# Performance work log

Measured on AMD Instinct MI355X. Metric: run time of the kernel, lower is better.

## Reference

```python
import jax, jax.numpy as jnp
import numpy as np

B, Q, K, QSIZE, KSIZE, H, VDIM = 4, 1024, 1024, 256, 256, 32, 256


def setup_inputs() -> dict:
    key = jax.random.key(0)
    ks = jax.random.split(key, 10)
    return {
        "keys": jax.random.normal(ks[0], (B, K, KSIZE), dtype=jnp.float32),
        "queries": jax.random.normal(ks[1], (B, Q, QSIZE), dtype=jnp.float32),
        "values": jax.random.normal(ks[2], (B, K, VDIM), dtype=jnp.float32),
        "valid_lens": jax.random.randint(ks[3], (B,), 1, K + 1, dtype=jnp.int32),
        "W_q": jax.random.normal(ks[4], (QSIZE, H), dtype=jnp.float32) * (QSIZE ** -0.5),
        "b_q": jnp.zeros((H,), dtype=jnp.float32),
        "W_k": jax.random.normal(ks[5], (KSIZE, H), dtype=jnp.float32) * (KSIZE ** -0.5),
        "b_k": jnp.zeros((H,), dtype=jnp.float32),
        "w_v": jax.random.normal(ks[6], (H,), dtype=jnp.float32) * (H ** -0.5),
        "b_v": jnp.zeros((), dtype=jnp.float32),
    }


def reference(keys, queries, values, valid_lens, W_q, b_q, W_k, b_k, w_v, b_v):
    # projected features: (B,K,H) and (B,Q,H)
    fk = keys @ W_k + b_k
    fq = queries @ W_q + b_q
    # broadcast add -> (B,Q,K,H), tanh, then scalar projection -> scores (B,Q,K)
    features = jnp.tanh(fq[:, :, None, :] + fk[:, None, :, :])
    scores = jnp.einsum("bqkh,h->bqk", features, w_v) + b_v
    # masked softmax over key axis: positions >= valid_len get -1e6
    mask = jnp.arange(K)[None, None, :] < valid_lens[:, None, None]
    scores = jnp.where(mask, scores, jnp.float32(-1e6))
    weights = jax.nn.softmax(scores, axis=-1)
    # bmm: (B,Q,K) @ (B,K,V) -> (B,Q,V)
    return jnp.einsum("bqk,bkv->bqv", weights, values)
```

## Files before the change

kernel.cpp:

```cpp
#include <hip/hip_runtime.h>
#include <math.h>


#define NB 4
#define NQ 1024
#define NK 1024
#define DQK 256
#define NH 32
#define NV 256
#define TQ 8
#define BLK 512

__device__ __forceinline__ float fast_rcp(float x) { return __builtin_amdgcn_rcpf(x); }

__global__ __launch_bounds__(256) void proj_kernel(
    const float* __restrict__ queries, const float* __restrict__ keys,
    const float* __restrict__ W_q, const float* __restrict__ b_q,
    const float* __restrict__ W_k, const float* __restrict__ b_k,
    float* __restrict__ eq, float* __restrict__ ek)
{
    const int tid     = blockIdx.x * 256 + threadIdx.x;
    const int row     = tid >> 5;
    const int sub     = tid & 31;
    const int h4      = (sub & 7) * 4;
    const int quarter = sub >> 3;

    const float* src; const float* W; const float* bias; float* dst; int r;
    if (row < NB * NQ) { r = row;           src = queries + (size_t)r * DQK; W = W_q; bias = b_q; dst = eq; }
    else               { r = row - NB * NQ; src = keys    + (size_t)r * DQK; W = W_k; bias = b_k; dst = ek; }

    float a0 = 0.f, a1 = 0.f, a2 = 0.f, a3 = 0.f;
    if (quarter == 0) {
        float4 bv4 = *(const float4*)(bias + h4);
        a0 = bv4.x; a1 = bv4.y; a2 = bv4.z; a3 = bv4.w;
    }
    const int d0 = quarter * 64;
    #pragma unroll 4
    for (int i = d0; i < d0 + 64; i += 4) {
        float4 s  = *(const float4*)(src + i);
        float4 w0 = *(const float4*)(W + (size_t)(i + 0) * NH + h4);
        float4 w1 = *(const float4*)(W + (size_t)(i + 1) * NH + h4);
        float4 w2 = *(const float4*)(W + (size_t)(i + 2) * NH + h4);
        float4 w3 = *(const float4*)(W + (size_t)(i + 3) * NH + h4);
        a0 = fmaf(s.x, w0.x, a0); a1 = fmaf(s.x, w0.y, a1); a2 = fmaf(s.x, w0.z, a2); a3 = fmaf(s.x, w0.w, a3);
        a0 = fmaf(s.y, w1.x, a0); a1 = fmaf(s.y, w1.y, a1); a2 = fmaf(s.y, w1.z, a2); a3 = fmaf(s.y, w1.w, a3);
        a0 = fmaf(s.z, w2.x, a0); a1 = fmaf(s.z, w2.y, a1); a2 = fmaf(s.z, w2.z, a2); a3 = fmaf(s.z, w2.w, a3);
        a0 = fmaf(s.w, w3.x, a0); a1 = fmaf(s.w, w3.y, a1); a2 = fmaf(s.w, w3.z, a2); a3 = fmaf(s.w, w3.w, a3);
    }
    a0 += __shfl_xor(a0, 8, 64);  a1 += __shfl_xor(a1, 8, 64);
    a2 += __shfl_xor(a2, 8, 64);  a3 += __shfl_xor(a3, 8, 64);
    a0 += __shfl_xor(a0, 16, 64); a1 += __shfl_xor(a1, 16, 64);
    a2 += __shfl_xor(a2, 16, 64); a3 += __shfl_xor(a3, 16, 64);
    if (quarter == 0) {
        float4 o;
        o.x = __expf(2.f * a0); o.y = __expf(2.f * a1);
        o.z = __expf(2.f * a2); o.w = __expf(2.f * a3);
        *(float4*)(dst + (size_t)r * NH + h4) = o;
    }
}

__global__ __launch_bounds__(BLK) void attn_kernel(
    const float* __restrict__ eq, const float* __restrict__ ek,
    const float* __restrict__ values, const int* __restrict__ valid_lens,
    const float* __restrict__ w_v, float* __restrict__ out)
{
    __shared__ float s_w[NK][TQ];
    __shared__ float s_part[8][TQ];

    const int t      = threadIdx.x;
    const int b      = blockIdx.x >> 7;
    const int q0     = (blockIdx.x & 127) * TQ;
    const int nvalid = valid_lens[b];
    const int wave   = t >> 6;
    const int lane   = t & 63;
    const int qi     = t & 7;
    const int ks     = t >> 3;

    float wv[NH];
    #pragma unroll
    for (int h = 0; h < NH; h += 4) {
        float4 w4 = *(const float4*)(w_v + h);
        wv[h] = w4.x; wv[h+1] = w4.y; wv[h+2] = w4.z; wv[h+3] = w4.w;
    }
    float eqr[NH];
    const float* eqp = eq + (size_t)(b * NQ + q0 + qi) * NH;
    #pragma unroll
    for (int h = 0; h < NH; h += 4) {
        float4 e4 = *(const float4*)(eqp + h);
        eqr[h] = e4.x; eqr[h+1] = e4.y; eqr[h+2] = e4.z; eqr[h+3] = e4.w;
    }

    const float* ekbase = ek + (size_t)b * NK * NH;
    const int imax = (nvalid + 63) >> 6;
    float ssum = 0.f;
    for (int i = 0; i < imax; i++) {
        const int k = ks + 64 * i;
        float e = 0.f;
        if (k < nvalid) {
            const float* ekp = ekbase + (size_t)k * NH;
            float acc = 0.f;
            #pragma unroll
            for (int h = 0; h < NH; h += 4) {
                float4 e4 = *(const float4*)(ekp + h);
                acc = fmaf(wv[h+0], fast_rcp(1.f + eqr[h+0] * e4.x), acc);
                acc = fmaf(wv[h+1], fast_rcp(1.f + eqr[h+1] * e4.y), acc);
                acc = fmaf(wv[h+2], fast_rcp(1.f + eqr[h+2] * e4.z), acc);
                acc = fmaf(wv[h+3], fast_rcp(1.f + eqr[h+3] * e4.w), acc);
            }
            e = __expf(-2.f * acc);
        }
        s_w[k][qi] = e;
        ssum += e;
    }

    ssum += __shfl_xor(ssum, 8, 64);
    ssum += __shfl_xor(ssum, 16, 64);
    ssum += __shfl_xor(ssum, 32, 64);
    if (lane < TQ) s_part[wave][lane] = ssum;
    __syncthreads();

    const int kpw  = (nvalid + 7) >> 3;
    const int kbeg = wave * kpw;
    const int kend = min(nvalid, kbeg + kpw);
    float4 acc0 = {0,0,0,0}, acc1 = {0,0,0,0}, acc2 = {0,0,0,0}, acc3 = {0,0,0,0};
    float4 acc4 = {0,0,0,0}, acc5 = {0,0,0,0}, acc6 = {0,0,0,0}, acc7 = {0,0,0,0};
    const float* vbase = values + (size_t)b * NK * NV + 4 * lane;

#define FMA4(A, W) A.x = fmaf((W), v.x, A.x); A.y = fmaf((W), v.y, A.y); \
                   A.z = fmaf((W), v.z, A.z); A.w = fmaf((W), v.w, A.w);
    #pragma unroll 2
    for (int k = kbeg; k < kend; k++) {
        float4 v  = *(const float4*)(vbase + (size_t)k * NV);
        float4 w0 = *(const float4*)(&s_w[k][0]);
        float4 w1 = *(const float4*)(&s_w[k][4]);
        FMA4(acc0, w0.x); FMA4(acc1, w0.y); FMA4(acc2, w0.z); FMA4(acc3, w0.w);
        FMA4(acc4, w1.x); FMA4(acc5, w1.y); FMA4(acc6, w1.z); FMA4(acc7, w1.w);
    }
#undef FMA4

    __syncthreads();
    float* sred = &s_w[0][0];
    float4* p = (float4*)(sred + (size_t)((wave & 3) * TQ) * 256) + lane;
    if (wave < 4) {
        p[0*64] = acc0; p[1*64] = acc1; p[2*64] = acc2; p[3*64] = acc3;
        p[4*64] = acc4; p[5*64] = acc5; p[6*64] = acc6; p[7*64] = acc7;
    }
    __syncthreads();
    if (wave >= 4) {
        float4 x;
#define ACC4(I, A) x = p[I*64]; x.x += A.x; x.y += A.y; x.z += A.z; x.w += A.w; p[I*64] = x;
        ACC4(0, acc0); ACC4(1, acc1); ACC4(2, acc2); ACC4(3, acc3);
        ACC4(4, acc4); ACC4(5, acc5); ACC4(6, acc6); ACC4(7, acc7);
#undef ACC4
    }
    __syncthreads();

    const int v  = t & 255;
    const int qh = (t >> 8) * 4;
    float* obase = out + (size_t)(b * NQ + q0) * NV + v;
    #pragma unroll
    for (int j = 0; j < 4; j++) {
        const int q = qh + j;
        float tot = 0.f;
        #pragma unroll
        for (int w = 0; w < 8; w++) tot += s_part[w][q];
        float rs = fast_rcp(tot);
        float r = sred[(0*TQ + q) * 256 + v] + sred[(1*TQ + q) * 256 + v]
                + sred[(2*TQ + q) * 256 + v] + sred[(3*TQ + q) * 256 + v];
        obase[(size_t)q * NV] = r * rs;
    }
}

extern "C" void kernel_launch(void* const* d_in, const int* in_sizes, int n_in,
                              void* d_out, int out_size, void* d_ws, size_t ws_size,
                              hipStream_t stream) {
    (void)in_sizes; (void)n_in; (void)out_size; (void)ws_size;
    const float* keys       = (const float*)d_in[0];
    const float* queries    = (const float*)d_in[1];
    const float* values     = (const float*)d_in[2];
    const int*   valid_lens = (const int*)d_in[3];
    const float* W_q        = (const float*)d_in[4];
    const float* b_q        = (const float*)d_in[5];
    const float* W_k        = (const float*)d_in[6];
    const float* b_k        = (const float*)d_in[7];
    const float* w_v        = (const float*)d_in[8];
    float* out = (float*)d_out;

    float* eq = (float*)d_ws;
    float* ek = eq + (size_t)NB * NQ * NH;

    proj_kernel<<<dim3(1024), dim3(256), 0, stream>>>(queries, keys, W_q, b_q, W_k, b_k, eq, ek);
    attn_kernel<<<dim3(NB * (NQ / TQ)), dim3(BLK), 0, stream>>>(eq, ek, values, valid_lens, w_v, out);
}
```

Measured before the change: 110.8 us.

## Combine tanh reciprocals pairwise and localize score computation per wave

Scores are now computed by each wave for exactly the key slice it later multiplies against values, which removes the block-wide barrier between scoring and the value accumulation. The sum of four w/(1+x) terms is rewritten as a single fraction so that only one reciprocal is needed per four hidden units, reducing transcendental throughput pressure. Launch bounds also request four blocks per CU, and the value loop is unrolled further. The combined-denominator form risks overflow or precision loss for large products, which is only partially guarded by a clamp.

```diff
diff --git a/kernel.cpp b/kernel.cpp
--- a/kernel.cpp
+++ b/kernel.cpp
@@ -59,7 +59,7 @@
     }
 }
 
-__global__ __launch_bounds__(BLK) void attn_kernel(
+__global__ __launch_bounds__(BLK, 4) void attn_kernel(
     const float* __restrict__ eq, const float* __restrict__ ek,
     const float* __restrict__ values, const int* __restrict__ valid_lens,
     const float* __restrict__ w_v, float* __restrict__ out)
@@ -73,8 +73,12 @@
     const int nvalid = valid_lens[b];
     const int wave   = t >> 6;
     const int lane   = t & 63;
-    const int qi     = t & 7;
-    const int ks     = t >> 3;
+    const int qi     = lane & 7;
+    const int kk     = lane >> 3;
+
+    const int kpw  = (nvalid + 7) >> 3;
+    const int kbeg = wave * kpw;
+    const int kend = min(nvalid, kbeg + kpw);
 
     float wv[NH];
     #pragma unroll
@@ -91,44 +95,44 @@
     }
 
     const float* ekbase = ek + (size_t)b * NK * NH;
-    const int imax = (nvalid + 63) >> 6;
     float ssum = 0.f;
-    for (int i = 0; i < imax; i++) {
-        const int k = ks + 64 * i;
-        float e = 0.f;
-        if (k < nvalid) {
+    for (int k0 = kbeg; k0 < kend; k0 += 8) {
+        const int k = k0 + kk;
+        if (k < kend) {
             const float* ekp = ekbase + (size_t)k * NH;
             float acc = 0.f;
             #pragma unroll
             for (int h = 0; h < NH; h += 4) {
                 float4 e4 = *(const float4*)(ekp + h);
-                acc = fmaf(wv[h+0], fast_rcp(1.f + eqr[h+0] * e4.x), acc);
-                acc = fmaf(wv[h+1], fast_rcp(1.f + eqr[h+1] * e4.y), acc);
-                acc = fmaf(wv[h+2], fast_rcp(1.f + eqr[h+2] * e4.z), acc);
-                acc = fmaf(wv[h+3], fast_rcp(1.f + eqr[h+3] * e4.w), acc);
+                float u0 = fmaf(eqr[h+0], e4.x, 1.f);
+                float u1 = fmaf(eqr[h+1], e4.y, 1.f);
+                float u2 = fmaf(eqr[h+2], e4.z, 1.f);
+                float u3 = fmaf(eqr[h+3], e4.w, 1.f);
+                float d01 = u0 * u1, d23 = u2 * u3;
+                float n01 = fmaf(wv[h+0], u1, wv[h+1] * u0);
+                float n23 = fmaf(wv[h+2], u3, wv[h+3] * u2);
+                float d   = fminf(d01 * d23, 1e38f);
+                float n   = fmaf(n01, d23, n23 * d01);
+                acc = fmaf(n, fast_rcp(d), acc);
             }
-            e = __expf(-2.f * acc);
+            float e = __expf(-2.f * acc);
+            s_w[k][qi] = e;
+            ssum += e;
         }
-        s_w[k][qi] = e;
-        ssum += e;
     }
 
     ssum += __shfl_xor(ssum, 8, 64);
     ssum += __shfl_xor(ssum, 16, 64);
     ssum += __shfl_xor(ssum, 32, 64);
     if (lane < TQ) s_part[wave][lane] = ssum;
-    __syncthreads();
 
-    const int kpw  = (nvalid + 7) >> 3;
-    const int kbeg = wave * kpw;
-    const int kend = min(nvalid, kbeg + kpw);
     float4 acc0 = {0,0,0,0}, acc1 = {0,0,0,0}, acc2 = {0,0,0,0}, acc3 = {0,0,0,0};
     float4 acc4 = {0,0,0,0}, acc5 = {0,0,0,0}, acc6 = {0,0,0,0}, acc7 = {0,0,0,0};
     const float* vbase = values + (size_t)b * NK * NV + 4 * lane;
 
 #define FMA4(A, W) A.x = fmaf((W), v.x, A.x); A.y = fmaf((W), v.y, A.y); \
                    A.z = fmaf((W), v.z, A.z); A.w = fmaf((W), v.w, A.w);
-    #pragma unroll 2
+    #pragma unroll 4
     for (int k = kbeg; k < kend; k++) {
         float4 v  = *(const float4*)(vbase + (size_t)k * NV);
         float4 w0 = *(const float4*)(&s_w[k][0]);
```

After: 107.7 us. 2.8% less time.
